# Kernel optimization log

Measured on AMD Instinct MI355X. Metric: run time of the kernel, lower is better.

Reference implementation:

```python
import jax, jax.numpy as jnp
import numpy as np

B, S, E, H, L = 32, 1024, 768, 64, 2  # batch, seq (<=1024 per bias buffer), embed, head hidden, labels
MASKED_BIAS = jnp.float32(-10000.0)


def setup_inputs() -> dict:
    key = jax.random.key(0)
    ks = jax.random.split(key, 12)
    s = 0.02  # init scale
    return {
        "hidden": jax.random.normal(ks[0], (B, S, E), dtype=jnp.float32),
        "attention_mask": jnp.ones((B, S), dtype=jnp.float32),
        # torch nn.Linear weights are [out, in]
        "Wk": jax.random.normal(ks[1], (E, E), dtype=jnp.float32) * s,
        "bk": jnp.zeros((E,), dtype=jnp.float32),
        "Wq": jax.random.normal(ks[2], (E, E), dtype=jnp.float32) * s,
        "bq": jnp.zeros((E,), dtype=jnp.float32),
        "Wv": jax.random.normal(ks[3], (E, E), dtype=jnp.float32) * s,
        "bv": jnp.zeros((E,), dtype=jnp.float32),
        "W1": jax.random.normal(ks[4], (H, E), dtype=jnp.float32) * s,
        "b1": jnp.zeros((H,), dtype=jnp.float32),
        "W2": jax.random.normal(ks[5], (L, H), dtype=jnp.float32) * s,
        "b2": jnp.zeros((L,), dtype=jnp.float32),
    }


def reference(hidden, attention_mask, Wk, bk, Wq, bq, Wv, bv, W1, b1, W2, b2):
    # Single-head causal attention, NO 1/sqrt(d) scaling (faithful to source).
    # Dropout layers run in eval mode -> identity.
    seq = hidden.shape[1]
    q = hidden @ Wq.T + bq            # [B,S,E]
    k = hidden @ Wk.T + bk            # [B,S,E]
    v = hidden @ Wv.T + bv            # [B,S,E] (v_drop is identity in eval)
    w = jnp.einsum('bqe,bke->bqk', q, k)  # [B,S,S]
    causal = jnp.tril(jnp.ones((seq, seq), dtype=bool))  # bias[:, ns-nd:ns, :ns] with nd==ns
    w = jnp.where(causal, w, MASKED_BIAS.astype(w.dtype))
    am = (1.0 - attention_mask)[:, None, :] * -10000.0    # [B,1,S]
    w = jax.nn.softmax(w + am, axis=-1)
    h = jnp.einsum('bqk,bke->bqe', w, v)  # [B,S,E]
    h = jax.nn.relu(h @ W1.T + b1)        # [B,S,64]
    return h @ W2.T + b2                  # [B,S,L]
```

## Files before the change

kernel.cpp:

```cpp
#include <hip/hip_runtime.h>
#include <hip/hip_bf16.h>
#include <cstdio>


typedef _Float16 f16;
typedef f16    f16x8 __attribute__((ext_vector_type(8)));
typedef f16    f16x4 __attribute__((ext_vector_type(4)));
typedef __bf16 bfx8  __attribute__((ext_vector_type(8)));
typedef float  f32x4 __attribute__((ext_vector_type(4)));

#define MFMA_F16(a,b,c)  __builtin_amdgcn_mfma_f32_16x16x32_f16((a),(b),(c),0,0,0)
#define MFMA_BF16(a,b,c) __builtin_amdgcn_mfma_f32_16x16x32_bf16((a),(b),(c),0,0,0)

static constexpr int LDT = 136;

__device__ __forceinline__ void gl_lds16(const void* g, void* l) {
    __builtin_amdgcn_global_load_lds(
        (const __attribute__((address_space(1))) void*)g,
        (__attribute__((address_space(3))) void*)l, 16, 0, 0);
}

__global__ __launch_bounds__(256) void cvt_all(
    const float* __restrict__ hidden,
    const float* __restrict__ Wq, const float* __restrict__ Wk, const float* __restrict__ Wv,
    f16* __restrict__ h16, f16* __restrict__ oq, f16* __restrict__ ok, f16* __restrict__ ov)
{
    const int bid = blockIdx.x;
    const float* src;
    f16* dst;
    int base;
    if (bid < 24576) {
        src = hidden; dst = h16;
        base = (bid * 256 + threadIdx.x) * 4;
    } else {
        int wz = (bid - 24576) / 576, wb = (bid - 24576) % 576;
        src = (wz == 0) ? Wq : (wz == 1) ? Wk : Wv;
        dst = (wz == 0) ? oq : (wz == 1) ? ok : ov;
        base = (wb * 256 + threadIdx.x) * 4;
    }
    f32x4 v = *(const f32x4*)(src + base);
    f16x4 o;
    #pragma unroll
    for (int e = 0; e < 4; ++e) o[e] = (f16)v[e];
    *(f16x4*)(dst + base) = o;
}

__global__ __launch_bounds__(256, 4) void qkv_kernel(
    const f16* __restrict__ h16,
    const f16* __restrict__ wq, const f16* __restrict__ wk, const f16* __restrict__ wv,
    const float* __restrict__ bq, const float* __restrict__ bk, const float* __restrict__ bv,
    f16* __restrict__ q16, f16* __restrict__ k16, __bf16* __restrict__ vT)
{
    const int f = blockIdx.x;
    const int xcd = f & 7;
    const int j = f >> 3;
    const int nt = j % 6;
    const int z  = (j / 6) % 3;
    const int mi = j / 18;
    const int mt = xcd + 8 * mi;
    const int m0 = mt * 128, n0 = nt * 128;

    const f16* W = (z == 0) ? wq : (z == 1) ? wk : wv;
    const float* bias = (z == 0) ? bq : (z == 1) ? bk : bv;

    __shared__ alignas(16) char smem[34816];
    f16 (*S)[8192] = (f16 (*)[8192])smem;
    __bf16* Tb = (__bf16*)smem;

    const int t = threadIdx.x, lane = t & 63, wave = t >> 6;
    const int wm = (wave & 1) * 64, wn = (wave >> 1) * 64;
    const int quad = lane >> 4, l16 = lane & 15;

    const f16* gsrc[4];
    int ldst[4];
    #pragma unroll
    for (int u = 0; u < 4; ++u) {
        int c = wave * 4 + u;
        ldst[u] = c * 512;
        int row = (c < 8) ? (m0 + c * 16 + l16) : (n0 + (c - 8) * 16 + l16);
        const f16* base = (c < 8) ? h16 : W;
        gsrc[u] = base + (size_t)row * 768 + quad * 8;
    }

    f32x4 acc[4][4] = {};
    auto stage = [&](int k0, int buf) {
        #pragma unroll
        for (int u = 0; u < 4; ++u)
            gl_lds16(gsrc[u] + k0, &S[buf][ldst[u]]);
    };
    auto compute = [&](int buf) {
        f16x8 af[4], bg[4];
        #pragma unroll
        for (int i = 0; i < 4; ++i) {
            af[i] = *(const f16x8*)&S[buf][(wm / 16 + i) * 512 + quad * 128 + l16 * 8];
            bg[i] = *(const f16x8*)&S[buf][(8 + wn / 16 + i) * 512 + quad * 128 + l16 * 8];
        }
        #pragma unroll
        for (int i = 0; i < 4; ++i)
            #pragma unroll
            for (int jj = 0; jj < 4; ++jj)
                acc[i][jj] = MFMA_F16(af[i], bg[jj], acc[i][jj]);
    };

    stage(0, 0);
    int cur = 0;
    for (int k0 = 32; k0 < 768; k0 += 32) {
        __syncthreads();
        stage(k0, cur ^ 1);
        compute(cur);
        cur ^= 1;
    }
    __syncthreads();
    compute(cur);

    if (z < 2) {
        f16* out = z ? k16 : q16;
        #pragma unroll
        for (int jj = 0; jj < 4; ++jj) {
            int col = n0 + wn + jj * 16 + l16;
            float bb = bias[col];
            #pragma unroll
            for (int i = 0; i < 4; ++i)
                #pragma unroll
                for (int r = 0; r < 4; ++r) {
                    int row = m0 + wm + i * 16 + quad * 4 + r;
                    out[(size_t)row * 768 + col] = (f16)(acc[i][jj][r] + bb);
                }
        }
    } else {
        __syncthreads();
        #pragma unroll
        for (int jj = 0; jj < 4; ++jj) {
            int el = wn + jj * 16 + l16;
            float bb = bias[n0 + el];
            #pragma unroll
            for (int i = 0; i < 4; ++i)
                #pragma unroll
                for (int r = 0; r < 4; ++r) {
                    int sl = wm + i * 16 + quad * 4 + r;
                    Tb[el * LDT + sl] = (__bf16)(acc[i][jj][r] + bb);
                }
        }
        __syncthreads();
        const int bofs = (m0 >> 10) * 768;
        const int s0 = m0 & 1023;
        const int ch = (t & 15) * 8;
        const int er = t >> 4;
        #pragma unroll
        for (int p = 0; p < 8; ++p) {
            int e = er + p * 16;
            bfx8 val = *(const bfx8*)&Tb[e * LDT + ch];
            *(bfx8*)&vT[(size_t)(bofs + n0 + e) * 1024 + s0 + ch] = val;
        }
    }
}

__global__ __launch_bounds__(256, 4) void logits_kernel(
    const f16* __restrict__ q16, const f16* __restrict__ k16,
    const float* __restrict__ amask, __bf16* __restrict__ pu, float* __restrict__ psum)
{
    const int f = blockIdx.x;
    const int xcd = f & 7;
    const int j = f >> 3;
    const int b = xcd + 8 * (j / 36);
    const int tile = j % 36;
    int mt = 0, base = 0;
    while (base + mt + 1 <= tile) { base += mt + 1; ++mt; }
    const int nt = tile - base;
    const int m0 = mt * 128, n0 = nt * 128;
    const size_t pb = (size_t)b << 20;
    const size_t qb = (size_t)b * 1024 * 768;

    __shared__ alignas(16) f16 S[2][8192];
    __shared__ float rs[2][128];

    const int t = threadIdx.x, lane = t & 63, wave = t >> 6;
    const int wm = (wave & 1) * 64, wn = (wave >> 1) * 64;
    const int quad = lane >> 4, l16 = lane & 15;

    const f16* gsrc[4];
    int ldst[4];
    #pragma unroll
    for (int u = 0; u < 4; ++u) {
        int c = wave * 4 + u;
        ldst[u] = c * 512;
        const f16* base2 = (c < 8) ? (q16 + qb + (size_t)(m0 + c * 16 + l16) * 768)
                                   : (k16 + qb + (size_t)(n0 + (c - 8) * 16 + l16) * 768);
        gsrc[u] = base2 + quad * 8;
    }

    f32x4 acc[4][4] = {};
    auto stage = [&](int k0, int buf) {
        #pragma unroll
        for (int u = 0; u < 4; ++u)
            gl_lds16(gsrc[u] + k0, &S[buf][ldst[u]]);
    };
    auto compute = [&](int buf) {
        f16x8 af[4], bg[4];
        #pragma unroll
        for (int i = 0; i < 4; ++i) {
            af[i] = *(const f16x8*)&S[buf][(wm / 16 + i) * 512 + quad * 128 + l16 * 8];
            bg[i] = *(const f16x8*)&S[buf][(8 + wn / 16 + i) * 512 + quad * 128 + l16 * 8];
        }
        #pragma unroll
        for (int i = 0; i < 4; ++i)
            #pragma unroll
            for (int jj = 0; jj < 4; ++jj)
                acc[i][jj] = MFMA_F16(af[i], bg[jj], acc[i][jj]);
    };

    stage(0, 0);
    int cur = 0;
    for (int k0 = 32; k0 < 768; k0 += 32) {
        __syncthreads();
        stage(k0, cur ^ 1);
        compute(cur);
        cur ^= 1;
    }
    __syncthreads();
    compute(cur);

    float rp[4][4] = {};
    #pragma unroll
    for (int jj = 0; jj < 4; ++jj) {
        int col = n0 + wn + jj * 16 + l16;
        float am = (1.0f - amask[b * 1024 + col]) * -10000.0f;
        #pragma unroll
        for (int i = 0; i < 4; ++i)
            #pragma unroll
            for (int r = 0; r < 4; ++r) {
                int row = m0 + wm + i * 16 + quad * 4 + r;
                float s = acc[i][jj][r] + am;
                float pval = (col <= row) ? __expf(fminf(s, 80.0f)) : 0.0f;
                pu[pb + (size_t)row * 1024 + col] = (__bf16)pval;
                rp[i][r] += pval;
            }
    }
    #pragma unroll
    for (int i = 0; i < 4; ++i)
        #pragma unroll
        for (int r = 0; r < 4; ++r) {
            float v = rp[i][r];
            v += __shfl_xor(v, 1, 64);
            v += __shfl_xor(v, 2, 64);
            v += __shfl_xor(v, 4, 64);
            v += __shfl_xor(v, 8, 64);
            if (l16 == 0) rs[wn >> 6][wm + i * 16 + quad * 4 + r] = v;
        }
    __syncthreads();
    if (t < 128)
        psum[((size_t)b * 1024 + m0 + t) * 8 + nt] = rs[0][t] + rs[1][t];
}

__global__ __launch_bounds__(256, 4) void pv_kernel(
    const __bf16* __restrict__ pu, const __bf16* __restrict__ vT,
    const float* __restrict__ psum, __bf16* __restrict__ h)
{
    const int f = blockIdx.x;
    const int xcd = f & 7;
    const int j = f >> 3;
    const int b = xcd + 8 * (j / 48);
    const int tile = j % 48;
    const int mt = 7 - tile / 6, nt = tile % 6;
    const int m0 = mt * 128, n0 = nt * 128;
    const size_t pb = (size_t)b << 20;
    const size_t vb = (size_t)b * 768 * 1024;

    __shared__ alignas(16) __bf16 S[2][8192];
    __shared__ float invl[128];

    const int t = threadIdx.x, lane = t & 63, wave = t >> 6;
    const int wm = (wave & 1) * 64, wn = (wave >> 1) * 64;
    const int quad = lane >> 4, l16 = lane & 15;

    if (t < 128) {
        int row = m0 + t;
        int lim = row >> 7;
        const float* pr = &psum[((size_t)b * 1024 + row) * 8];
        float s = 0.f;
        #pragma unroll
        for (int n = 0; n < 8; ++n) s += (n <= lim) ? pr[n] : 0.f;
        invl[t] = 1.0f / s;
    }

    const __bf16* gsrc[4];
    int ldst[4];
    #pragma unroll
    for (int u = 0; u < 4; ++u) {
        int c = wave * 4 + u;
        ldst[u] = c * 512;
        const __bf16* base = (c < 8) ? (pu + pb + (size_t)(m0 + c * 16 + l16) * 1024)
                                     : (vT + vb + (size_t)(n0 + (c - 8) * 16 + l16) * 1024);
        gsrc[u] = base + quad * 8;
    }

    f32x4 acc[4][4] = {};
    auto stage = [&](int k0, int buf) {
        #pragma unroll
        for (int u = 0; u < 4; ++u)
            gl_lds16(gsrc[u] + k0, &S[buf][ldst[u]]);
    };
    auto compute = [&](int buf) {
        bfx8 af[4], bg[4];
        #pragma unroll
        for (int i = 0; i < 4; ++i) {
            af[i] = *(const bfx8*)&S[buf][(wm / 16 + i) * 512 + quad * 128 + l16 * 8];
            bg[i] = *(const bfx8*)&S[buf][(8 + wn / 16 + i) * 512 + quad * 128 + l16 * 8];
        }
        #pragma unroll
        for (int i = 0; i < 4; ++i)
            #pragma unroll
            for (int jj = 0; jj < 4; ++jj)
                acc[i][jj] = MFMA_BF16(af[i], bg[jj], acc[i][jj]);
    };

    const int kend = m0 + 128;
    stage(0, 0);
    int cur = 0;
    for (int k0 = 32; k0 < kend; k0 += 32) {
        __syncthreads();
        stage(k0, cur ^ 1);
        compute(cur);
        cur ^= 1;
    }
    __syncthreads();
    compute(cur);

    #pragma unroll
    for (int jj = 0; jj < 4; ++jj) {
        int col = n0 + wn + jj * 16 + l16;
        #pragma unroll
        for (int i = 0; i < 4; ++i)
            #pragma unroll
            for (int r = 0; r < 4; ++r) {
                int rl = wm + i * 16 + quad * 4 + r;
                h[((size_t)b * 1024 + m0 + rl) * 768 + col] = (__bf16)(acc[i][jj][r] * invl[rl]);
            }
    }
}

__global__ __launch_bounds__(256) void mlp_kernel(
    const __bf16* __restrict__ h, const float* __restrict__ W1, const float* __restrict__ b1,
    const float* __restrict__ W2, const float* __restrict__ b2, float* __restrict__ out)
{
    const int wave = threadIdx.x >> 6, lane = threadIdx.x & 63;
    const int quad = lane >> 4, l16 = lane & 15;
    const int m0 = blockIdx.x * 64 + wave * 16;

    f32x4 acc[4] = {};
    for (int k0 = 0; k0 < 768; k0 += 32) {
        bfx8 af = *(const bfx8*)&h[(size_t)(m0 + l16) * 768 + k0 + quad * 8];
        #pragma unroll
        for (int jj = 0; jj < 4; ++jj) {
            const float* wp = W1 + (size_t)(jj * 16 + l16) * 768 + k0 + quad * 8;
            f32x4 w0 = *(const f32x4*)wp;
            f32x4 w1 = *(const f32x4*)(wp + 4);
            bfx8 bg;
            #pragma unroll
            for (int e = 0; e < 4; ++e) { bg[e] = (__bf16)w0[e]; bg[e + 4] = (__bf16)w1[e]; }
            acc[jj] = MFMA_BF16(af, bg, acc[jj]);
        }
    }
    float part[4][2] = {};
    #pragma unroll
    for (int jj = 0; jj < 4; ++jj) {
        int c = jj * 16 + l16;
        float bb = b1[c];
        float w20 = W2[c], w21 = W2[64 + c];
        #pragma unroll
        for (int r = 0; r < 4; ++r) {
            float x = fmaxf(acc[jj][r] + bb, 0.f);
            part[r][0] += x * w20;
            part[r][1] += x * w21;
        }
    }
    #pragma unroll
    for (int off = 1; off < 16; off <<= 1)
        #pragma unroll
        for (int r = 0; r < 4; ++r) {
            part[r][0] += __shfl_xor(part[r][0], off, 64);
            part[r][1] += __shfl_xor(part[r][1], off, 64);
        }
    if (l16 == 0) {
        #pragma unroll
        for (int r = 0; r < 4; ++r) {
            int row = m0 + quad * 4 + r;
            out[(size_t)row * 2 + 0] = part[r][0] + b2[0];
            out[(size_t)row * 2 + 1] = part[r][1] + b2[1];
        }
    }
}

extern "C" void kernel_launch(void* const* d_in, const int* in_sizes, int n_in,
                              void* d_out, int out_size, void* d_ws, size_t ws_size,
                              hipStream_t stream)
{
    const float* hidden = (const float*)d_in[0];
    const float* amask  = (const float*)d_in[1];
    const float* Wk = (const float*)d_in[2];
    const float* bk = (const float*)d_in[3];
    const float* Wq = (const float*)d_in[4];
    const float* bq = (const float*)d_in[5];
    const float* Wv = (const float*)d_in[6];
    const float* bv = (const float*)d_in[7];
    const float* W1 = (const float*)d_in[8];
    const float* b1 = (const float*)d_in[9];
    const float* W2 = (const float*)d_in[10];
    const float* b2 = (const float*)d_in[11];
    float* out = (float*)d_out;

    char* ws = (char*)d_ws;
    const size_t MB = 1024 * 1024;
    f16* h16 = (f16*)ws;
    f16* wq16 = (f16*)(ws + 48 * MB);
    f16* wk16 = wq16 + 589824;
    f16* wv16 = wk16 + 589824;
    __bf16* pu  = (__bf16*)ws;
    float*  psum = (float*)(ws + 64 * MB);
    f16* q16 = (f16*)(ws + 66 * MB);
    f16* k16 = (f16*)(ws + 114 * MB);
    __bf16* vT = (__bf16*)(ws + 162 * MB);
    __bf16* h  = (__bf16*)(ws + 66 * MB);
    const size_t NEED = 210 * MB;
    if (ws_size < NEED) {
        fprintf(stderr, "[Attn kernel] ws too small: %zu < %zu — skipping launches\n",
                ws_size, NEED);
        return;
    }

    cvt_all<<<24576 + 1728, 256, 0, stream>>>(
        hidden, Wq, Wk, Wv, h16, wq16, wk16, wv16);

    qkv_kernel<<<4608, 256, 0, stream>>>(
        h16, wq16, wk16, wv16, bq, bk, bv, q16, k16, vT);
    logits_kernel<<<1152, 256, 0, stream>>>(q16, k16, amask, pu, psum);
    pv_kernel<<<1536, 256, 0, stream>>>(pu, vT, psum, h);
    mlp_kernel<<<512, 256, 0, stream>>>(h, W1, b1, W2, b2, out);
}
```

Measured before the change: 571.1 us.

## Enlarge QKV GEMM tiles to 256x256 with 8 waves and phased prefetch

Measured after the change: 519.7 us. 1.1x faster.

```diff
diff --git a/kernel.cpp b/kernel.cpp
--- a/kernel.cpp
+++ b/kernel.cpp
@@ -12,13 +12,15 @@
 #define MFMA_F16(a,b,c)  __builtin_amdgcn_mfma_f32_16x16x32_f16((a),(b),(c),0,0,0)
 #define MFMA_BF16(a,b,c) __builtin_amdgcn_mfma_f32_16x16x32_bf16((a),(b),(c),0,0,0)
 
-static constexpr int LDT = 136;
+static constexpr int LDT2 = 264;
 
 __device__ __forceinline__ void gl_lds16(const void* g, void* l) {
     __builtin_amdgcn_global_load_lds(
         (const __attribute__((address_space(1))) void*)g,
         (__attribute__((address_space(3))) void*)l, 16, 0, 0);
 }
+
+#define S_BARRIER()  asm volatile("s_barrier" ::: "memory")
 
 __global__ __launch_bounds__(256) void cvt_all(
     const float* __restrict__ hidden,
@@ -45,7 +47,32 @@
     *(f16x4*)(dst + base) = o;
 }
 
-__global__ __launch_bounds__(256, 4) void qkv_kernel(
+#define QPHASE(fr0, STAGE_STMT, GATE_STMT)                                        \
+    {                                                                             \
+        f16x8 afr[2][2];                                                          \
+        _Pragma("unroll")                                                         \
+        for (int i = 0; i < 2; ++i) {                                             \
+            _Pragma("unroll")                                                     \
+            for (int kk = 0; kk < 2; ++kk)                                        \
+                afr[i][kk] = *(const f16x8*)&SA[kk * 8192 + (wr8 + (fr0) + i) * 512 + lq]; \
+        }                                                                         \
+        STAGE_STMT;                                                               \
+        GATE_STMT;                                                                \
+        S_BARRIER();                                                              \
+        __builtin_amdgcn_s_setprio(1);                                            \
+        _Pragma("unroll")                                                         \
+        for (int i = 0; i < 2; ++i) {                                             \
+            _Pragma("unroll")                                                     \
+            for (int jj = 0; jj < 4; ++jj) {                                      \
+                acc[(fr0) + i][jj] = MFMA_F16(afr[i][0], bfr[jj][0], acc[(fr0) + i][jj]); \
+                acc[(fr0) + i][jj] = MFMA_F16(afr[i][1], bfr[jj][1], acc[(fr0) + i][jj]); \
+            }                                                                     \
+        }                                                                         \
+        __builtin_amdgcn_s_setprio(0);                                            \
+        S_BARRIER();                                                              \
+    }
+
+__global__ __launch_bounds__(512, 2) void qkv_kernel(
     const f16* __restrict__ h16,
     const f16* __restrict__ wq, const f16* __restrict__ wk, const f16* __restrict__ wv,
     const float* __restrict__ bq, const float* __restrict__ bk, const float* __restrict__ bv,
@@ -54,103 +81,114 @@
     const int f = blockIdx.x;
     const int xcd = f & 7;
     const int j = f >> 3;
-    const int nt = j % 6;
-    const int z  = (j / 6) % 3;
-    const int mi = j / 18;
+    const int nt = j % 3;
+    const int z  = (j / 3) % 3;
+    const int mi = j / 9;
     const int mt = xcd + 8 * mi;
-    const int m0 = mt * 128, n0 = nt * 128;
+    const int m0 = mt * 256, n0 = nt * 256;
 
     const f16* W = (z == 0) ? wq : (z == 1) ? wk : wv;
     const float* bias = (z == 0) ? bq : (z == 1) ? bk : bv;
 
-    __shared__ alignas(16) char smem[34816];
-    f16 (*S)[8192] = (f16 (*)[8192])smem;
-    __bf16* Tb = (__bf16*)smem;
+    __shared__ alignas(16) f16 S[65536];
 
     const int t = threadIdx.x, lane = t & 63, wave = t >> 6;
-    const int wm = (wave & 1) * 64, wn = (wave >> 1) * 64;
+    const int wr = wave >> 2, wc = wave & 3;
+    const int wr8 = wr * 8;
     const int quad = lane >> 4, l16 = lane & 15;
-
-    const f16* gsrc[4];
-    int ldst[4];
-    #pragma unroll
-    for (int u = 0; u < 4; ++u) {
-        int c = wave * 4 + u;
-        ldst[u] = c * 512;
-        int row = (c < 8) ? (m0 + c * 16 + l16) : (n0 + (c - 8) * 16 + l16);
-        const f16* base = (c < 8) ? h16 : W;
-        gsrc[u] = base + (size_t)row * 768 + quad * 8;
-    }
-
-    f32x4 acc[4][4] = {};
-    auto stage = [&](int k0, int buf) {
-        #pragma unroll
-        for (int u = 0; u < 4; ++u)
-            gl_lds16(gsrc[u] + k0, &S[buf][ldst[u]]);
+    const int lq = quad * 128 + l16 * 8;
+
+    const f16* gA = h16 + (size_t)(m0 + l16) * 768 + quad * 8;
+    const f16* gB = W   + (size_t)(n0 + l16) * 768 + quad * 8;
+    int gofs[2], lofs[2];
+    #pragma unroll
+    for (int u = 0; u < 2; ++u) {
+        int unit = wave * 2 + u;
+        int kk = unit >> 3, c = unit & 7;
+        gofs[u] = c * 16 * 768 + kk * 32;
+        lofs[u] = kk * 8192 + c * 512;
+    }
+    auto stage = [&](int kt, int mat, int half) {
+        const f16* gp = (mat ? gB : gA) + half * (128 * 768) + kt * 64;
+        f16* lp = &S[(kt & 1) * 32768 + mat * 16384 + half * 4096];
+        gl_lds16(gp + gofs[0], lp + lofs[0]);
+        gl_lds16(gp + gofs[1], lp + lofs[1]);
     };
-    auto compute = [&](int buf) {
-        f16x8 af[4], bg[4];
-        #pragma unroll
-        for (int i = 0; i < 4; ++i) {
-            af[i] = *(const f16x8*)&S[buf][(wm / 16 + i) * 512 + quad * 128 + l16 * 8];
-            bg[i] = *(const f16x8*)&S[buf][(8 + wn / 16 + i) * 512 + quad * 128 + l16 * 8];
-        }
-        #pragma unroll
-        for (int i = 0; i < 4; ++i)
-            #pragma unroll
-            for (int jj = 0; jj < 4; ++jj)
-                acc[i][jj] = MFMA_F16(af[i], bg[jj], acc[i][jj]);
-    };
-
-    stage(0, 0);
-    int cur = 0;
-    for (int k0 = 32; k0 < 768; k0 += 32) {
-        __syncthreads();
-        stage(k0, cur ^ 1);
-        compute(cur);
-        cur ^= 1;
-    }
-    __syncthreads();
-    compute(cur);
+
+    f32x4 acc[8][4] = {};
+
+    stage(0, 0, 0); stage(0, 0, 1); stage(0, 1, 0); stage(0, 1, 1);
+    stage(1, 1, 0); stage(1, 1, 1);
+    asm volatile("s_waitcnt vmcnt(4)" ::: "memory");
+    S_BARRIER();
+
+    f16x8 bfr[4][2];
+    for (int kt = 0; kt < 12; ++kt) {
+        const f16* SA = &S[(kt & 1) * 32768];
+        const f16* SB = SA + 16384;
+        #pragma unroll
+        for (int jj = 0; jj < 4; ++jj) {
+            #pragma unroll
+            for (int kk = 0; kk < 2; ++kk)
+                bfr[jj][kk] = *(const f16x8*)&SB[kk * 8192 + (wc * 4 + jj) * 512 + lq];
+        }
+        QPHASE(0, { if (kt + 1 < 12) stage(kt + 1, 0, 0); }, {});
+        QPHASE(2, { if (kt + 1 < 12) stage(kt + 1, 0, 1); }, {});
+        QPHASE(4, { if (kt + 2 < 12) stage(kt + 2, 1, 0); }, {});
+        QPHASE(6, { if (kt + 2 < 12) stage(kt + 2, 1, 1); },
+               {
+                   if (kt + 2 < 12)       asm volatile("s_waitcnt vmcnt(4)" ::: "memory");
+                   else if (kt + 1 < 12)  asm volatile("s_waitcnt vmcnt(0)" ::: "memory");
+               });
+    }
 
     if (z < 2) {
         f16* out = z ? k16 : q16;
         #pragma unroll
         for (int jj = 0; jj < 4; ++jj) {
-            int col = n0 + wn + jj * 16 + l16;
+            int col = n0 + wc * 64 + jj * 16 + l16;
             float bb = bias[col];
             #pragma unroll
-            for (int i = 0; i < 4; ++i)
+            for (int fi = 0; fi < 8; ++fi) {
                 #pragma unroll
                 for (int r = 0; r < 4; ++r) {
-                    int row = m0 + wm + i * 16 + quad * 4 + r;
-                    out[(size_t)row * 768 + col] = (f16)(acc[i][jj][r] + bb);
+                    int row = m0 + wr * 128 + fi * 16 + quad * 4 + r;
+                    out[(size_t)row * 768 + col] = (f16)(acc[fi][jj][r] + bb);
                 }
+            }
         }
     } else {
-        __syncthreads();
-        #pragma unroll
-        for (int jj = 0; jj < 4; ++jj) {
-            int el = wn + jj * 16 + l16;
-            float bb = bias[n0 + el];
-            #pragma unroll
-            for (int i = 0; i < 4; ++i)
-                #pragma unroll
-                for (int r = 0; r < 4; ++r) {
-                    int sl = wm + i * 16 + quad * 4 + r;
-                    Tb[el * LDT + sl] = (__bf16)(acc[i][jj][r] + bb);
-                }
-        }
-        __syncthreads();
+        __bf16* Tb = (__bf16*)S;
+        const int halfw = wc >> 1;
         const int bofs = (m0 >> 10) * 768;
         const int s0 = m0 & 1023;
-        const int ch = (t & 15) * 8;
-        const int er = t >> 4;
-        #pragma unroll
-        for (int p = 0; p < 8; ++p) {
-            int e = er + p * 16;
-            bfx8 val = *(const bfx8*)&Tb[e * LDT + ch];
-            *(bfx8*)&vT[(size_t)(bofs + n0 + e) * 1024 + s0 + ch] = val;
+        #pragma unroll
+        for (int half = 0; half < 2; ++half) {
+            __syncthreads();
+            if (halfw == half) {
+                #pragma unroll
+                for (int jj = 0; jj < 4; ++jj) {
+                    int el = (wc & 1) * 64 + jj * 16 + l16;
+                    float bb = bias[n0 + half * 128 + el];
+                    #pragma unroll
+                    for (int fi = 0; fi < 8; ++fi) {
+                        #pragma unroll
+                        for (int r = 0; r < 4; ++r) {
+                            int sl = wr * 128 + fi * 16 + quad * 4 + r;
+                            Tb[el * LDT2 + sl] = (__bf16)(acc[fi][jj][r] + bb);
+                        }
+                    }
+                }
+            }
+            __syncthreads();
+            const int ch = (t & 31) * 8;
+            const int rbase = t >> 5;
+            #pragma unroll
+            for (int p = 0; p < 8; ++p) {
+                int e = rbase + p * 16;
+                bfx8 val = *(const bfx8*)&Tb[e * LDT2 + ch];
+                *(bfx8*)&vT[(size_t)(bofs + n0 + half * 128 + e) * 1024 + s0 + ch] = val;
+            }
         }
     }
 }
@@ -431,7 +469,7 @@
     cvt_all<<<24576 + 1728, 256, 0, stream>>>(
         hidden, Wq, Wk, Wv, h16, wq16, wk16, wv16);
 
-    qkv_kernel<<<4608, 256, 0, stream>>>(
+    qkv_kernel<<<1152, 512, 0, stream>>>(
         h16, wq16, wk16, wv16, bq, bk, bv, q16, k16, vT);
     logits_kernel<<<1152, 256, 0, stream>>>(q16, k16, amask, pu, psum);
     pv_kernel<<<1536, 256, 0, stream>>>(pu, vT, psum, h);
```
